# Kernel tuning notes

Hardware: AMD Instinct MI355X
Metric: run time of the kernel (lower is better)

Reference implementation:

```python
import jax, jax.numpy as jnp
import numpy as np

BN_EPS = 1e-5


def setup_inputs() -> dict:
    key = jax.random.key(0)
    ks = jax.random.split(key, 12)
    B, D, N, M, H = 8, 3, 20000, 1024, 1024
    x = jax.random.normal(ks[0], (B, D, N), dtype=jnp.float32)
    # random basis points inside a unit ball (as bps.generate_random_basis)
    dirs = jax.random.normal(ks[1], (M, D), dtype=jnp.float32)
    dirs = dirs / jnp.linalg.norm(dirs, axis=1, keepdims=True)
    r = jax.random.uniform(ks[2], (M, 1), dtype=jnp.float32) ** (1.0 / 3.0)
    basis = dirs * r
    return {
        "x": x,
        "basis": basis,
        "bn1_g": jax.random.uniform(ks[3], (M,), dtype=jnp.float32) + 0.5,
        "bn1_b": jax.random.normal(ks[4], (M,), dtype=jnp.float32) * 0.1,
        "bn1_rm": jax.random.normal(ks[5], (M,), dtype=jnp.float32) * 0.1,
        "bn1_rv": jax.random.uniform(ks[6], (M,), dtype=jnp.float32) + 0.5,
        "w1": jax.random.normal(ks[7], (H, M), dtype=jnp.float32) * (1.0 / np.sqrt(M)),
        "b1": jnp.zeros((H,), dtype=jnp.float32),
        "bn2_g": jax.random.uniform(ks[8], (H,), dtype=jnp.float32) + 0.5,
        "bn2_b": jax.random.normal(ks[9], (H,), dtype=jnp.float32) * 0.1,
        "bn2_rm": jax.random.normal(ks[10], (H,), dtype=jnp.float32) * 0.1,
        "bn2_rv": jax.random.uniform(ks[11], (H,), dtype=jnp.float32) + 0.5,
        "w2": jax.random.normal(jax.random.fold_in(key, 99), (1, H), dtype=jnp.float32) * (1.0 / np.sqrt(H)),
        "b2": jnp.zeros((1,), dtype=jnp.float32),
    }


def _bps_encode(x, basis):
    # x: [B, 3, N]; basis: [M, 3] -> sqrt(min_n ||p_n - b_m||^2): [B, M]
    pts = jnp.transpose(x, (0, 2, 1))                      # [B, N, 3]
    x2 = jnp.sum(pts * pts, axis=-1)                       # [B, N]
    b2 = jnp.sum(basis * basis, axis=-1)                   # [M]
    cross = jnp.einsum('bnd,md->bnm', pts, basis)          # [B, N, M]
    dist2 = x2[:, :, None] + b2[None, None, :] - 2.0 * cross
    dist2 = jnp.clip(dist2, 0.0, None)
    return jnp.sqrt(jnp.min(dist2, axis=1))                # [B, M]


def _bn_eval(f, g, b, rm, rv):
    return (f - rm) * (g / jnp.sqrt(rv + BN_EPS)) + b


def reference(x, basis, bn1_g, bn1_b, bn1_rm, bn1_rv, w1, b1,
              bn2_g, bn2_b, bn2_rm, bn2_rv, w2, b2):
    f = _bps_encode(x, basis)                              # [B, M]
    f = _bn_eval(f, bn1_g, bn1_b, bn1_rm, bn1_rv)
    f = f @ w1.T + b1                                      # [B, 1024]
    f = jax.nn.relu(f)
    f = _bn_eval(f, bn2_g, bn2_b, bn2_rm, bn2_rv)
    # Dropout(p=0.8) is identity in eval mode
    out = f @ w2.T + b2                                    # [B, 1]
    return out
```

## Files before the change

### kernel.cpp

```cpp
#include <hip/hip_runtime.h>
#include <hip/hip_bf16.h>
#include <math.h>

#define B 8
#define NPTS 20000
#define M 1024
#define H 1024
#define BN_EPS 1e-5f

#define BPS_CHUNK 160
#define BPS_NCHUNK 125
#define KM 16

typedef float f2 __attribute__((ext_vector_type(2)));

__global__ __launch_bounds__(256) void bps_kernel(const float* __restrict__ x,
                                                  const float* __restrict__ basis,
                                                  unsigned int* __restrict__ fmin) {
    __shared__ f2 sx[BPS_CHUNK / 2], sy[BPS_CHUNK / 2], sz[BPS_CHUNK / 2], sw[BPS_CHUNK / 2];
    __shared__ float smin[4][M];
    const int chunk = blockIdx.x;
    const int b = blockIdx.y;
    const int tid = threadIdx.x;
    const int lane = tid & 63;
    const int w = tid >> 6;
    const int n0 = chunk * BPS_CHUNK;
    const float* xb = x + (size_t)b * 3 * NPTS;

    if (tid < BPS_CHUNK) {
        float px = xb[n0 + tid];
        float py = xb[NPTS + n0 + tid];
        float pz = xb[2 * NPTS + n0 + tid];
        ((float*)sx)[tid] = px;
        ((float*)sy)[tid] = py;
        ((float*)sz)[tid] = pz;
        ((float*)sw)[tid] = px * px + py * py + pz * pz;
    }

    float nbx[KM], nby[KM], nbz[KM], bb2[KM];
#pragma unroll
    for (int i = 0; i < KM; ++i) {
        int m = lane + 64 * i;
        float bx = basis[m * 3 + 0];
        float by = basis[m * 3 + 1];
        float bz = basis[m * 3 + 2];
        nbx[i] = -2.0f * bx;
        nby[i] = -2.0f * by;
        nbz[i] = -2.0f * bz;
        bb2[i] = bx * bx + by * by + bz * bz;
    }
    float acc[KM];
#pragma unroll
    for (int i = 0; i < KM; ++i) acc[i] = INFINITY;
    __syncthreads();

    const int j0 = w * (BPS_CHUNK / 8);
#pragma unroll 2
    for (int j = j0; j < j0 + BPS_CHUNK / 8; ++j) {
        f2 X = sx[j];
        f2 Y = sy[j];
        f2 Z = sz[j];
        f2 W = sw[j];
#pragma unroll
        for (int i = 0; i < KM; ++i) {
            f2 s = __builtin_elementwise_fma(X, (f2){nbx[i], nbx[i]}, W);
            s = __builtin_elementwise_fma(Y, (f2){nby[i], nby[i]}, s);
            s = __builtin_elementwise_fma(Z, (f2){nbz[i], nbz[i]}, s);
            acc[i] = fminf(acc[i], fminf(s.x, s.y));
        }
    }

#pragma unroll
    for (int i = 0; i < KM; ++i) {
        smin[w][lane + 64 * i] = acc[i] + bb2[i];
    }
    __syncthreads();

#pragma unroll
    for (int q = 0; q < 4; ++q) {
        int m = tid + q * 256;
        float v = fminf(fminf(smin[0][m], smin[1][m]), fminf(smin[2][m], smin[3][m]));
        v = fmaxf(v, 0.0f);
        atomicMin(&fmin[b * M + m], __float_as_uint(v));
    }
}

__global__ __launch_bounds__(256) void mlp_kernel(const unsigned int* __restrict__ fmin,
                                                  const float* __restrict__ g1,
                                                  const float* __restrict__ bb1,
                                                  const float* __restrict__ rm1,
                                                  const float* __restrict__ rv1,
                                                  const float* __restrict__ w1,
                                                  const float* __restrict__ b1,
                                                  const float* __restrict__ g2,
                                                  const float* __restrict__ bb2v,
                                                  const float* __restrict__ rm2,
                                                  const float* __restrict__ rv2,
                                                  const float* __restrict__ w2,
                                                  float* __restrict__ psum) {
    __shared__ float fs[B * M];
    const int tid = threadIdx.x;

    for (int e = tid; e < B * M; e += 256) {
        int m = e & (M - 1);
        float f = sqrtf(__uint_as_float(fmin[e]));
        float sc = g1[m] * rsqrtf(rv1[m] + BN_EPS);
        fs[e] = (f - rm1[m]) * sc + bb1[m];
    }
    __syncthreads();

    const int lane = tid & 63;
    const int wv = tid >> 6;
    const int i = blockIdx.x * 4 + wv;
    const float* wrow = w1 + (size_t)i * M;

    float hsum[B] = {0, 0, 0, 0, 0, 0, 0, 0};
#pragma unroll
    for (int seg = 0; seg < 4; ++seg) {
        int m0 = seg * 256 + lane * 4;
        float4 wv4 = *reinterpret_cast<const float4*>(wrow + m0);
#pragma unroll
        for (int bb = 0; bb < B; ++bb) {
            float4 fv = *reinterpret_cast<const float4*>(&fs[bb * M + m0]);
            hsum[bb] = fmaf(fv.x, wv4.x, hsum[bb]);
            hsum[bb] = fmaf(fv.y, wv4.y, hsum[bb]);
            hsum[bb] = fmaf(fv.z, wv4.z, hsum[bb]);
            hsum[bb] = fmaf(fv.w, wv4.w, hsum[bb]);
        }
    }
#pragma unroll
    for (int bb = 0; bb < B; ++bb) {
#pragma unroll
        for (int off = 32; off > 0; off >>= 1) {
            hsum[bb] += __shfl_down(hsum[bb], off, 64);
        }
    }
    if (lane == 0) {
        float b1i = b1[i];
        float sc2 = g2[i] * rsqrtf(rv2[i] + BN_EPS);
        float rm = rm2[i];
        float bt = bb2v[i];
        float w2i = w2[i];
#pragma unroll
        for (int bb = 0; bb < B; ++bb) {
            float v = fmaxf(hsum[bb] + b1i, 0.0f);
            v = (v - rm) * sc2 + bt;
            psum[(size_t)i * B + bb] = v * w2i;
        }
    }
}

__global__ __launch_bounds__(256) void out_kernel(const float* __restrict__ psum,
                                                  const float* __restrict__ b2,
                                                  float* __restrict__ out) {
    const int tid = threadIdx.x;
    const int bb = tid >> 5;
    const int sl = tid & 31;
    float s = 0.0f;
    for (int i = sl; i < H; i += 32) {
        s += psum[(size_t)i * B + bb];
    }
#pragma unroll
    for (int off = 16; off > 0; off >>= 1) {
        s += __shfl_down(s, off, 32);
    }
    if (sl == 0) {
        out[bb] = s + b2[0];
    }
}

extern "C" void kernel_launch(void* const* d_in, const int* in_sizes, int n_in,
                              void* d_out, int out_size, void* d_ws, size_t ws_size,
                              hipStream_t stream) {
    const float* x      = (const float*)d_in[0];
    const float* basis  = (const float*)d_in[1];
    const float* bn1_g  = (const float*)d_in[2];
    const float* bn1_b  = (const float*)d_in[3];
    const float* bn1_rm = (const float*)d_in[4];
    const float* bn1_rv = (const float*)d_in[5];
    const float* w1     = (const float*)d_in[6];
    const float* b1     = (const float*)d_in[7];
    const float* bn2_g  = (const float*)d_in[8];
    const float* bn2_b  = (const float*)d_in[9];
    const float* bn2_rm = (const float*)d_in[10];
    const float* bn2_rv = (const float*)d_in[11];
    const float* w2     = (const float*)d_in[12];
    const float* b2     = (const float*)d_in[13];
    float* out = (float*)d_out;

    unsigned int* fmin = (unsigned int*)d_ws;
    float* psum = (float*)((char*)d_ws + (size_t)B * M * 4);

    hipMemsetAsync(fmin, 0x7F, (size_t)B * M * 4, stream);

    dim3 g1g(BPS_NCHUNK, B);
    bps_kernel<<<g1g, 256, 0, stream>>>(x, basis, fmin);

    mlp_kernel<<<H / 4, 256, 0, stream>>>(fmin, bn1_g, bn1_b, bn1_rm, bn1_rv, w1, b1,
                                          bn2_g, bn2_b, bn2_rm, bn2_rv, w2, psum);

    out_kernel<<<1, 256, 0, stream>>>(psum, b2, out);
}
```

Before: 49.43 us.

## Fuse BPS encode, MLP and output into one cooperative kernel with grid syncs

Replaces the memset plus three kernel launches with a single cooperative kernel of 256 blocks. The stages are separated by grid.sync, and the atomicMin reduction is replaced by per-slab partial minima that are reduced deterministically afterwards. Each block now handles 625 points with float4 shared loads, which cuts launch overhead and atomics. In exchange it adds three grid-wide barriers, a larger shared memory footprint of about 62KB per block, and fewer blocks (256 rather than 1000) for the distance stage.

```diff
diff --git a/kernel.cpp b/kernel.cpp
--- a/kernel.cpp
+++ b/kernel.cpp
@@ -1,6 +1,8 @@
 #include <hip/hip_runtime.h>
-#include <hip/hip_bf16.h>
+#include <hip/hip_cooperative_groups.h>
 #include <math.h>
+
+namespace cg = cooperative_groups;
 
 #define B 8
 #define NPTS 20000
@@ -8,196 +10,212 @@
 #define H 1024
 #define BN_EPS 1e-5f
 
-#define BPS_CHUNK 160
-#define BPS_NCHUNK 125
+#define NSLAB 32
+#define SLABPTS 625
 #define KM 16
 
 typedef float f2 __attribute__((ext_vector_type(2)));
 
-__global__ __launch_bounds__(256) void bps_kernel(const float* __restrict__ x,
-                                                  const float* __restrict__ basis,
-                                                  unsigned int* __restrict__ fmin) {
-    __shared__ f2 sx[BPS_CHUNK / 2], sy[BPS_CHUNK / 2], sz[BPS_CHUNK / 2], sw[BPS_CHUNK / 2];
+struct Params {
+    const float *x, *basis;
+    const float *g1, *bb1, *rm1, *rv1;
+    const float *w1, *b1;
+    const float *g2, *bb2, *rm2, *rv2;
+    const float *w2, *b2;
+    float *out;
+    float *pmin;
+    float *fsg;
+    float *psum;
+};
+
+__global__ __launch_bounds__(256) void fused_kernel(Params p) {
+    __shared__ float sxf[626], syf[626], szf[626], swf[626];
     __shared__ float smin[4][M];
-    const int chunk = blockIdx.x;
-    const int b = blockIdx.y;
+    __shared__ float fsl[B * M];
+    cg::grid_group grid = cg::this_grid();
+    const int bid = blockIdx.x;
     const int tid = threadIdx.x;
     const int lane = tid & 63;
     const int w = tid >> 6;
-    const int n0 = chunk * BPS_CHUNK;
-    const float* xb = x + (size_t)b * 3 * NPTS;
-
-    if (tid < BPS_CHUNK) {
-        float px = xb[n0 + tid];
-        float py = xb[NPTS + n0 + tid];
-        float pz = xb[2 * NPTS + n0 + tid];
-        ((float*)sx)[tid] = px;
-        ((float*)sy)[tid] = py;
-        ((float*)sz)[tid] = pz;
-        ((float*)sw)[tid] = px * px + py * py + pz * pz;
-    }
-
-    float nbx[KM], nby[KM], nbz[KM], bb2[KM];
-#pragma unroll
-    for (int i = 0; i < KM; ++i) {
-        int m = lane + 64 * i;
-        float bx = basis[m * 3 + 0];
-        float by = basis[m * 3 + 1];
-        float bz = basis[m * 3 + 2];
-        nbx[i] = -2.0f * bx;
-        nby[i] = -2.0f * by;
-        nbz[i] = -2.0f * bz;
-        bb2[i] = bx * bx + by * by + bz * bz;
-    }
-    float acc[KM];
-#pragma unroll
-    for (int i = 0; i < KM; ++i) acc[i] = INFINITY;
-    __syncthreads();
-
-    const int j0 = w * (BPS_CHUNK / 8);
-#pragma unroll 2
-    for (int j = j0; j < j0 + BPS_CHUNK / 8; ++j) {
-        f2 X = sx[j];
-        f2 Y = sy[j];
-        f2 Z = sz[j];
-        f2 W = sw[j];
+
+    {
+        const int b = bid >> 5;
+        const int slab = bid & 31;
+        const int n0 = slab * SLABPTS;
+        const float* xb = p.x + (size_t)b * 3 * NPTS;
+
+        for (int idx = tid; idx < SLABPTS; idx += 256) {
+            float px = xb[n0 + idx];
+            float py = xb[NPTS + n0 + idx];
+            float pz = xb[2 * NPTS + n0 + idx];
+            sxf[idx] = px;
+            syf[idx] = py;
+            szf[idx] = pz;
+            swf[idx] = px * px + py * py + pz * pz;
+        }
+
+        float nbx[KM], nby[KM], nbz[KM], bb2r[KM], acc[KM];
 #pragma unroll
         for (int i = 0; i < KM; ++i) {
-            f2 s = __builtin_elementwise_fma(X, (f2){nbx[i], nbx[i]}, W);
-            s = __builtin_elementwise_fma(Y, (f2){nby[i], nby[i]}, s);
-            s = __builtin_elementwise_fma(Z, (f2){nbz[i], nbz[i]}, s);
-            acc[i] = fminf(acc[i], fminf(s.x, s.y));
-        }
-    }
-
-#pragma unroll
-    for (int i = 0; i < KM; ++i) {
-        smin[w][lane + 64 * i] = acc[i] + bb2[i];
-    }
-    __syncthreads();
-
-#pragma unroll
-    for (int q = 0; q < 4; ++q) {
-        int m = tid + q * 256;
-        float v = fminf(fminf(smin[0][m], smin[1][m]), fminf(smin[2][m], smin[3][m]));
-        v = fmaxf(v, 0.0f);
-        atomicMin(&fmin[b * M + m], __float_as_uint(v));
-    }
-}
-
-__global__ __launch_bounds__(256) void mlp_kernel(const unsigned int* __restrict__ fmin,
-                                                  const float* __restrict__ g1,
-                                                  const float* __restrict__ bb1,
-                                                  const float* __restrict__ rm1,
-                                                  const float* __restrict__ rv1,
-                                                  const float* __restrict__ w1,
-                                                  const float* __restrict__ b1,
-                                                  const float* __restrict__ g2,
-                                                  const float* __restrict__ bb2v,
-                                                  const float* __restrict__ rm2,
-                                                  const float* __restrict__ rv2,
-                                                  const float* __restrict__ w2,
-                                                  float* __restrict__ psum) {
-    __shared__ float fs[B * M];
-    const int tid = threadIdx.x;
-
-    for (int e = tid; e < B * M; e += 256) {
+            int m = lane + 64 * i;
+            float bx = p.basis[m * 3 + 0];
+            float by = p.basis[m * 3 + 1];
+            float bz = p.basis[m * 3 + 2];
+            nbx[i] = -2.0f * bx;
+            nby[i] = -2.0f * by;
+            nbz[i] = -2.0f * bz;
+            bb2r[i] = bx * bx + by * by + bz * bz;
+            acc[i] = INFINITY;
+        }
+        __syncthreads();
+
+        const int j0 = w * 78;
+        for (int j = j0; j < j0 + 78; j += 2) {
+            float4 X4 = *reinterpret_cast<float4*>(&sxf[2 * j]);
+            float4 Y4 = *reinterpret_cast<float4*>(&syf[2 * j]);
+            float4 Z4 = *reinterpret_cast<float4*>(&szf[2 * j]);
+            float4 W4 = *reinterpret_cast<float4*>(&swf[2 * j]);
+            f2 Xa = {X4.x, X4.y}, Xb = {X4.z, X4.w};
+            f2 Ya = {Y4.x, Y4.y}, Yb = {Y4.z, Y4.w};
+            f2 Za = {Z4.x, Z4.y}, Zb = {Z4.z, Z4.w};
+            f2 Wa = {W4.x, W4.y}, Wb = {W4.z, W4.w};
+#pragma unroll
+            for (int i = 0; i < KM; ++i) {
+                f2 s0 = __builtin_elementwise_fma(Xa, (f2){nbx[i], nbx[i]}, Wa);
+                s0 = __builtin_elementwise_fma(Ya, (f2){nby[i], nby[i]}, s0);
+                s0 = __builtin_elementwise_fma(Za, (f2){nbz[i], nbz[i]}, s0);
+                f2 s1 = __builtin_elementwise_fma(Xb, (f2){nbx[i], nbx[i]}, Wb);
+                s1 = __builtin_elementwise_fma(Yb, (f2){nby[i], nby[i]}, s1);
+                s1 = __builtin_elementwise_fma(Zb, (f2){nbz[i], nbz[i]}, s1);
+                acc[i] = fminf(acc[i], fminf(fminf(s0.x, s0.y), fminf(s1.x, s1.y)));
+            }
+        }
+        if (w == 0) {
+            float px = sxf[624], py = syf[624], pz = szf[624], pw = swf[624];
+#pragma unroll
+            for (int i = 0; i < KM; ++i) {
+                float s = fmaf(px, nbx[i], pw);
+                s = fmaf(py, nby[i], s);
+                s = fmaf(pz, nbz[i], s);
+                acc[i] = fminf(acc[i], s);
+            }
+        }
+
+#pragma unroll
+        for (int i = 0; i < KM; ++i) smin[w][lane + 64 * i] = acc[i] + bb2r[i];
+        __syncthreads();
+
+#pragma unroll
+        for (int q = 0; q < 4; ++q) {
+            int m = tid + q * 256;
+            float v = fminf(fminf(smin[0][m], smin[1][m]), fminf(smin[2][m], smin[3][m]));
+            p.pmin[(size_t)slab * (B * M) + b * M + m] = fmaxf(v, 0.0f);
+        }
+    }
+    grid.sync();
+
+    if (bid < 32) {
+        int e = bid * 256 + tid;
         int m = e & (M - 1);
-        float f = sqrtf(__uint_as_float(fmin[e]));
-        float sc = g1[m] * rsqrtf(rv1[m] + BN_EPS);
-        fs[e] = (f - rm1[m]) * sc + bb1[m];
-    }
-    __syncthreads();
-
-    const int lane = tid & 63;
-    const int wv = tid >> 6;
-    const int i = blockIdx.x * 4 + wv;
-    const float* wrow = w1 + (size_t)i * M;
-
-    float hsum[B] = {0, 0, 0, 0, 0, 0, 0, 0};
-#pragma unroll
-    for (int seg = 0; seg < 4; ++seg) {
-        int m0 = seg * 256 + lane * 4;
-        float4 wv4 = *reinterpret_cast<const float4*>(wrow + m0);
+        float v = INFINITY;
+#pragma unroll 8
+        for (int s = 0; s < NSLAB; ++s) {
+            v = fminf(v, p.pmin[(size_t)s * (B * M) + e]);
+        }
+        float f = sqrtf(v);
+        float sc = p.g1[m] * rsqrtf(p.rv1[m] + BN_EPS);
+        p.fsg[e] = (f - p.rm1[m]) * sc + p.bb1[m];
+    }
+    grid.sync();
+
+    {
+        for (int k = tid; k < B * M / 4; k += 256) {
+            reinterpret_cast<float4*>(fsl)[k] = reinterpret_cast<const float4*>(p.fsg)[k];
+        }
+        __syncthreads();
+
+        const int i = bid * 4 + w;
+        const float* wrow = p.w1 + (size_t)i * M;
+        float hsum[B] = {0, 0, 0, 0, 0, 0, 0, 0};
+#pragma unroll
+        for (int seg = 0; seg < 4; ++seg) {
+            int m0 = seg * 256 + lane * 4;
+            float4 wv4 = *reinterpret_cast<const float4*>(wrow + m0);
+#pragma unroll
+            for (int bb = 0; bb < B; ++bb) {
+                float4 fv = *reinterpret_cast<const float4*>(&fsl[bb * M + m0]);
+                hsum[bb] = fmaf(fv.x, wv4.x, hsum[bb]);
+                hsum[bb] = fmaf(fv.y, wv4.y, hsum[bb]);
+                hsum[bb] = fmaf(fv.z, wv4.z, hsum[bb]);
+                hsum[bb] = fmaf(fv.w, wv4.w, hsum[bb]);
+            }
+        }
 #pragma unroll
         for (int bb = 0; bb < B; ++bb) {
-            float4 fv = *reinterpret_cast<const float4*>(&fs[bb * M + m0]);
-            hsum[bb] = fmaf(fv.x, wv4.x, hsum[bb]);
-            hsum[bb] = fmaf(fv.y, wv4.y, hsum[bb]);
-            hsum[bb] = fmaf(fv.z, wv4.z, hsum[bb]);
-            hsum[bb] = fmaf(fv.w, wv4.w, hsum[bb]);
-        }
-    }
-#pragma unroll
-    for (int bb = 0; bb < B; ++bb) {
-#pragma unroll
-        for (int off = 32; off > 0; off >>= 1) {
-            hsum[bb] += __shfl_down(hsum[bb], off, 64);
-        }
-    }
-    if (lane == 0) {
-        float b1i = b1[i];
-        float sc2 = g2[i] * rsqrtf(rv2[i] + BN_EPS);
-        float rm = rm2[i];
-        float bt = bb2v[i];
-        float w2i = w2[i];
-#pragma unroll
-        for (int bb = 0; bb < B; ++bb) {
-            float v = fmaxf(hsum[bb] + b1i, 0.0f);
-            v = (v - rm) * sc2 + bt;
-            psum[(size_t)i * B + bb] = v * w2i;
-        }
-    }
-}
-
-__global__ __launch_bounds__(256) void out_kernel(const float* __restrict__ psum,
-                                                  const float* __restrict__ b2,
-                                                  float* __restrict__ out) {
-    const int tid = threadIdx.x;
-    const int bb = tid >> 5;
-    const int sl = tid & 31;
-    float s = 0.0f;
-    for (int i = sl; i < H; i += 32) {
-        s += psum[(size_t)i * B + bb];
-    }
-#pragma unroll
-    for (int off = 16; off > 0; off >>= 1) {
-        s += __shfl_down(s, off, 32);
-    }
-    if (sl == 0) {
-        out[bb] = s + b2[0];
+#pragma unroll
+            for (int off = 32; off > 0; off >>= 1) {
+                hsum[bb] += __shfl_down(hsum[bb], off, 64);
+            }
+        }
+        if (lane == 0) {
+            float b1i = p.b1[i];
+            float sc2 = p.g2[i] * rsqrtf(p.rv2[i] + BN_EPS);
+            float rm = p.rm2[i];
+            float bt = p.bb2[i];
+            float w2i = p.w2[i];
+#pragma unroll
+            for (int bb = 0; bb < B; ++bb) {
+                float v = fmaxf(hsum[bb] + b1i, 0.0f);
+                v = (v - rm) * sc2 + bt;
+                p.psum[(size_t)i * B + bb] = v * w2i;
+            }
+        }
+    }
+    grid.sync();
+
+    if (bid == 0) {
+        const int bb = tid >> 5;
+        const int sl = tid & 31;
+        float s = 0.0f;
+        for (int i = sl; i < H; i += 32) {
+            s += p.psum[(size_t)i * B + bb];
+        }
+#pragma unroll
+        for (int off = 16; off > 0; off >>= 1) {
+            s += __shfl_down(s, off, 32);
+        }
+        if (sl == 0) {
+            p.out[bb] = s + p.b2[0];
+        }
     }
 }
 
 extern "C" void kernel_launch(void* const* d_in, const int* in_sizes, int n_in,
                               void* d_out, int out_size, void* d_ws, size_t ws_size,
                               hipStream_t stream) {
-    const float* x      = (const float*)d_in[0];
-    const float* basis  = (const float*)d_in[1];
-    const float* bn1_g  = (const float*)d_in[2];
-    const float* bn1_b  = (const float*)d_in[3];
-    const float* bn1_rm = (const float*)d_in[4];
-    const float* bn1_rv = (const float*)d_in[5];
-    const float* w1     = (const float*)d_in[6];
-    const float* b1     = (const float*)d_in[7];
-    const float* bn2_g  = (const float*)d_in[8];
-    const float* bn2_b  = (const float*)d_in[9];
-    const float* bn2_rm = (const float*)d_in[10];
-    const float* bn2_rv = (const float*)d_in[11];
-    const float* w2     = (const float*)d_in[12];
-    const float* b2     = (const float*)d_in[13];
-    float* out = (float*)d_out;
-
-    unsigned int* fmin = (unsigned int*)d_ws;
-    float* psum = (float*)((char*)d_ws + (size_t)B * M * 4);
-
-    hipMemsetAsync(fmin, 0x7F, (size_t)B * M * 4, stream);
-
-    dim3 g1g(BPS_NCHUNK, B);
-    bps_kernel<<<g1g, 256, 0, stream>>>(x, basis, fmin);
-
-    mlp_kernel<<<H / 4, 256, 0, stream>>>(fmin, bn1_g, bn1_b, bn1_rm, bn1_rv, w1, b1,
-                                          bn2_g, bn2_b, bn2_rm, bn2_rv, w2, psum);
-
-    out_kernel<<<1, 256, 0, stream>>>(psum, b2, out);
+    Params prm;
+    prm.x     = (const float*)d_in[0];
+    prm.basis = (const float*)d_in[1];
+    prm.g1    = (const float*)d_in[2];
+    prm.bb1   = (const float*)d_in[3];
+    prm.rm1   = (const float*)d_in[4];
+    prm.rv1   = (const float*)d_in[5];
+    prm.w1    = (const float*)d_in[6];
+    prm.b1    = (const float*)d_in[7];
+    prm.g2    = (const float*)d_in[8];
+    prm.bb2   = (const float*)d_in[9];
+    prm.rm2   = (const float*)d_in[10];
+    prm.rv2   = (const float*)d_in[11];
+    prm.w2    = (const float*)d_in[12];
+    prm.b2    = (const float*)d_in[13];
+    prm.out   = (float*)d_out;
+
+    char* ws = (char*)d_ws;
+    prm.pmin = (float*)ws;
+    prm.fsg  = (float*)(ws + (size_t)NSLAB * B * M * 4);
+    prm.psum = (float*)(ws + (size_t)NSLAB * B * M * 4 + B * M * 4);
+
+    void* args[] = { &prm };
+    hipLaunchCooperativeKernel((const void*)fused_kernel, dim3(256), dim3(256),
+                               args, 0, stream);
 }
```

Result: slower. 134.9 us (+172.9%).
